# Performance work log

Measured on AMD Instinct MI355X. Metric: run time of the kernel, lower is better.

## Reference

```python
import jax, jax.numpy as jnp
import numpy as np

B, V, K, DIN, H, DH, OBS, HID = 2048, 3, 32, 256, 8, 64, 128, 256
REP = H * DH
EPS = 1e-6


def _ln(x, g, b):
    mu = x.mean(-1, keepdims=True)
    var = ((x - mu) ** 2).mean(-1, keepdims=True)
    return (x - mu) * jax.lax.rsqrt(var + 1e-5) * g + b


def setup_inputs() -> dict:
    key = jax.random.key(0)
    ks = iter(jax.random.split(key, 32))
    nrm = lambda shape, s=0.05: jax.random.normal(next(ks), shape, jnp.float32) * s
    return {
        'x_anchor': jax.random.normal(next(ks), (B, V, DIN), jnp.float32),
        'x_neighbors': jax.random.normal(next(ks), (B, V, K, DIN), jnp.float32),
        'edge_weights': jax.random.uniform(next(ks), (B, V, K), jnp.float32),
        'g': jax.random.normal(next(ks), (B, OBS), jnp.float32),
        'aW': nrm((V, DIN, REP)), 'ab': jnp.zeros((V, REP)), 'ag': jnp.ones((V, REP)), 'abeta': jnp.zeros((V, REP)),
        'nW': nrm((V, DIN, REP)), 'nb': jnp.zeros((V, REP)), 'ng': jnp.ones((V, REP)), 'nbeta': jnp.zeros((V, REP)),
        'Wq': nrm((V, H, DH, DH)), 'Wk': nrm((V, H, DH, DH)), 'Wv': nrm((V, H, DH, DH)), 'Wo': nrm((V, H, DH, DH)),
        'geom_log_scale': jnp.zeros((V, H)),
        'cWq': nrm((H, DH, DH)), 'cWk': nrm((H, DH, DH)), 'cWv': nrm((H, DH, DH)), 'cWo': nrm((H, DH, DH)),
        'rW1': nrm((OBS, HID)), 'rb1': jnp.zeros((HID,)),
        'rW2': nrm((HID, HID)), 'rb2': jnp.zeros((HID,)),
        'vW': nrm((HID, H * V)), 'vb': jnp.zeros((H * V,)),
        'mW': nrm((HID, H)), 'mb': jnp.zeros((H,)),
        'gW': nrm((HID, H)), 'gb': jnp.zeros((H,)),
    }


def reference(x_anchor, x_neighbors, edge_weights, g, aW, ab, ag, abeta, nW, nb, ng, nbeta,
              Wq, Wk, Wv, Wo, geom_log_scale, cWq, cWk, cWv, cWo,
              rW1, rb1, rW2, rb2, vW, vb, mW, mb, gW, gb):
    # --- per-view encoders (vectorized over V with a leading v axis) ---
    ha = _ln(jnp.einsum('bvi,vio->bvo', x_anchor, aW) + ab, ag, abeta).reshape(B, V, H, DH)
    hn = _ln(jnp.einsum('bvki,vio->bvko', x_neighbors, nW) + nb[:, None, :],
             ng[:, None, :], nbeta[:, None, :]).reshape(B, V, K, H, DH)
    q = jnp.einsum('bvhd,vhde->bvhe', ha, Wq)
    k = jnp.einsum('bvkhd,vhde->bvkhe', hn, Wk)
    vv = jnp.einsum('bvkhd,vhde->bvkhe', hn, Wv)
    sc = jnp.einsum('bvhd,bvkhd->bvhk', q, k) / np.sqrt(DH).astype(np.float32)
    geom = jax.nn.softplus(geom_log_scale)  # [V,H]
    sc = sc + geom[None, :, :, None] * jnp.log(edge_weights[:, :, None, :] + EPS)
    attn = jax.nn.softmax(sc, axis=-1)
    ho = jnp.einsum('bvhk,bvkhd->bvhd', attn, vv)
    ho = jnp.einsum('bvhd,vhde->bvhe', ho, Wo) + ha  # residual
    view_tokens = jnp.transpose(ho, (0, 2, 1, 3))  # [B,H,V,Dh]
    # --- router ---
    hid = jax.nn.gelu(jnp.dot(g, rW1) + rb1, approximate=False)
    hid = jax.nn.gelu(jnp.dot(hid, rW2) + rb2, approximate=False)
    pi = jax.nn.softmax((jnp.dot(hid, vW) + vb).reshape(B, H, V), axis=-1)
    beta = jax.nn.sigmoid((jnp.dot(hid, mW) + mb)[..., None])  # [B,H,1]
    gate = jax.nn.softmax(jnp.dot(hid, gW) + gb, axis=-1)      # [B,H]
    # --- pi-weighted mixture + cross-view interaction with log-pi prior ---
    mix = jnp.einsum('bhv,bhvd->bhd', pi, view_tokens)
    qc = jnp.einsum('bhd,hde->bhe', mix, cWq)
    kc = jnp.einsum('bhvd,hde->bhve', view_tokens, cWk)
    vc = jnp.einsum('bhvd,hde->bhve', view_tokens, cWv)
    s2 = jnp.einsum('bhd,bhvd->bhv', qc, kc) / np.sqrt(DH).astype(np.float32) + jnp.log(pi + EPS)
    a2 = jax.nn.softmax(s2, axis=-1)
    cr = jnp.einsum('bhv,bhvd->bhd', a2, vc)
    cr = jnp.einsum('bhd,hde->bhe', cr, cWo)
    # mode blend + head gating; head_repr kept unflattened [B,H,Dh]
    return gate[..., None] * (beta * cr + (1.0 - beta) * mix)
```

## Files before the change

kernel.cpp:

```cpp
#include <hip/hip_runtime.h>

#define B_   2048
#define V_   3
#define K_   32
#define DIN_ 256
#define H_   8
#define DH_  64
#define REP_ 512

typedef unsigned short u16;
typedef unsigned int   u32;
typedef __bf16 bf8 __attribute__((ext_vector_type(8)));
typedef float  f4  __attribute__((ext_vector_type(4)));

static __device__ __forceinline__ u16 f2bf(float f) {
  union { float f; u32 i; } x; x.f = f;
  u32 r = (x.i + 0x7FFFu + ((x.i >> 16) & 1u)) >> 16;
  return (u16)r;
}
static __device__ __forceinline__ float bf2f(u16 u) {
  union { u32 i; float f; } x; x.i = ((u32)u) << 16;
  return x.f;
}
static __device__ __forceinline__ float bflo(u32 q) {
  union { u32 i; float f; } x; x.i = q << 16; return x.f;
}
static __device__ __forceinline__ float bfhi(u32 q) {
  union { u32 i; float f; } x; x.i = q & 0xffff0000u; return x.f;
}

static __device__ __forceinline__ void gl2lds16(const u16* g, u16* l) {
  __builtin_amdgcn_global_load_lds(
      (const __attribute__((address_space(1))) unsigned int*)(g),
      (__attribute__((address_space(3))) unsigned int*)(l), 16, 0, 0);
}

__global__ __launch_bounds__(256) void k0_prep(
    const float* __restrict__ nW, const float* __restrict__ aW,
    const float* __restrict__ Wv,
    u16* __restrict__ nWt, u16* __restrict__ aWt,
    u16* __restrict__ Wvt)
{
  int id = blockIdx.x * 256 + threadIdx.x;
  if (id < 393216) {
    int v  = id / 131072, r  = id % 131072;
    int kt = r / 16384,   r2 = r % 16384;
    int n  = r2 >> 5;
    int s  = (r2 >> 3) & 3;
    int m  = r2 & 7;
    int c  = s ^ ((n >> 1) & 3);
    int k  = kt * 32 + c * 8 + m;
    int src = (v * 256 + k) * 512 + n;
    nWt[id] = f2bf(nW[src]);
    aWt[id] = f2bf(aW[src]);
  } else {
    int j = id - 393216;
    int vh = j / 4096, r = j % 4096;
    int e = r / 64, d = r % 64;
    int src = (vh * 64 + d) * 64 + e;
    Wvt[j] = f2bf(Wv[src]);
  }
}

__global__ __launch_bounds__(256) void k0_wqk(
    const float* __restrict__ Wq, const float* __restrict__ Wk,
    float* __restrict__ Wqk)
{
  int vh = blockIdx.x, t = threadIdx.x;
  __shared__ float wq[4096], wkT[4096];
  #pragma unroll
  for (int i = 0; i < 16; ++i) {
    int idx = i * 256 + t;
    wq[idx] = Wq[(long)vh * 4096 + idx];
    int e = idx >> 6, c = idx & 63;
    wkT[c * 64 + e] = Wk[(long)vh * 4096 + e * 64 + c];
  }
  __syncthreads();
  int d = t >> 2, e0 = (t & 3) * 16;
  float acc[16];
  #pragma unroll
  for (int j = 0; j < 16; ++j) acc[j] = 0.f;
  for (int c = 0; c < 64; ++c) {
    float a = wq[d * 64 + c];
    const float* wr = &wkT[c * 64 + e0];
    #pragma unroll
    for (int j = 0; j < 16; ++j) acc[j] += a * wr[j];
  }
  #pragma unroll
  for (int j = 0; j < 16; ++j) Wqk[(long)vh * 4096 + d * 64 + e0 + j] = acc[j];
}

union K1Smem {
  struct { u16 A[64 * 256]; u16 B[16384]; } p;
  u16 S[64 * 512];
};

__global__ __launch_bounds__(512, 4) void k1_gemm_ln(
    const float* __restrict__ X,
    const u16*   __restrict__ Wt,
    const float* __restrict__ bias,
    const float* __restrict__ gamma,
    const float* __restrict__ betap,
    u16*   __restrict__ hn,
    float* __restrict__ ha,
    int mode, int b0, int Bc)
{
  __shared__ K1Smem sm;
  const int v = blockIdx.y, blk = blockIdx.x, t = threadIdx.x;
  const int w = t >> 6, l = t & 63, lm = l & 15, lg = l >> 4;
  const int wm = w & 1, wn = w >> 1;

  float bcol[8];
  #pragma unroll
  for (int tn = 0; tn < 8; ++tn) bcol[tn] = bias[v * 512 + wn * 128 + tn * 16 + lm];

  {
    int row = t >> 3;
    int cbase = (t & 7) * 32;
    long grow;
    if (mode == 0) { int b = b0 + blk * 2 + (row >> 5); grow = ((long)(b * 3 + v) * 32 + (row & 31)) * 256; }
    else           { int b = blk * 64 + row;            grow = (long)(b * 3 + v) * 256; }
    const float4* src = (const float4*)(X + grow + cbase);
    int sw = row & 7;
    #pragma unroll
    for (int j = 0; j < 8; ++j) {
      float4 f = src[j];
      int col = cbase + j * 4;
      int c = col >> 3, m = col & 7;
      ushort4 u;
      u.x = f2bf(f.x); u.y = f2bf(f.y); u.z = f2bf(f.z); u.w = f2bf(f.w);
      *(ushort4*)&sm.p.A[row * 256 + ((c ^ sw) << 3) + m] = u;
    }
  }

  f4 acc[2][8];
  #pragma unroll
  for (int i = 0; i < 2; ++i)
    #pragma unroll
    for (int j = 0; j < 8; ++j) { f4 z = {0.f, 0.f, 0.f, 0.f}; acc[i][j] = z; }

  const u16* Wbase = Wt + (long)v * 8 * 16384;
  for (int kt = 0; kt < 8; ++kt) {
    __syncthreads();
    {
      const u16* gp = Wbase + (long)kt * 16384 + t * 8;
      u16* lp = &sm.p.B[t * 8];
      #pragma unroll
      for (int r = 0; r < 4; ++r) gl2lds16(gp + r * 4096, lp + r * 4096);
    }
    __syncthreads();
    bf8 af[2];
    #pragma unroll
    for (int tm = 0; tm < 2; ++tm) {
      int row = wm * 32 + tm * 16 + lm;
      int c = kt * 4 + lg;
      af[tm] = *(const bf8*)&sm.p.A[row * 256 + ((c ^ (row & 7)) << 3)];
    }
    #pragma unroll
    for (int tn = 0; tn < 8; ++tn) {
      int n = wn * 128 + tn * 16 + lm;
      bf8 bv = *(const bf8*)&sm.p.B[n * 32 + ((lg ^ ((n >> 1) & 3)) << 3)];
      acc[0][tn] = __builtin_amdgcn_mfma_f32_16x16x32_bf16(af[0], bv, acc[0][tn], 0, 0, 0);
      acc[1][tn] = __builtin_amdgcn_mfma_f32_16x16x32_bf16(af[1], bv, acc[1][tn], 0, 0, 0);
    }
  }
  __syncthreads();

  #pragma unroll
  for (int tm = 0; tm < 2; ++tm)
    #pragma unroll
    for (int tn = 0; tn < 8; ++tn) {
      int col = wn * 128 + tn * 16 + lm;
      int c = col >> 3, m = col & 7;
      #pragma unroll
      for (int r = 0; r < 4; ++r) {
        int row = wm * 32 + tm * 16 + lg * 4 + r;
        sm.S[row * 512 + ((c ^ (row & 7)) << 3) + m] = f2bf(acc[tm][tn][r] + bcol[tn]);
      }
    }
  __syncthreads();

  {
    int row = t >> 3, ch = t & 7, sw = row & 7;
    float s1 = 0.f, s2 = 0.f;
    #pragma unroll
    for (int j = 0; j < 8; ++j) {
      int c = j * 8 + ch;
      uint4 q = *(const uint4*)&sm.S[row * 512 + ((c ^ sw) << 3)];
      float x0 = bflo(q.x), x1 = bfhi(q.x), x2 = bflo(q.y), x3 = bfhi(q.y);
      float x4 = bflo(q.z), x5 = bfhi(q.z), x6 = bflo(q.w), x7 = bfhi(q.w);
      s1 += ((x0 + x1) + (x2 + x3)) + ((x4 + x5) + (x6 + x7));
      s2 += ((x0*x0 + x1*x1) + (x2*x2 + x3*x3)) + ((x4*x4 + x5*x5) + (x6*x6 + x7*x7));
    }
    #pragma unroll
    for (int d = 1; d < 8; d <<= 1) { s1 += __shfl_xor(s1, d, 64); s2 += __shfl_xor(s2, d, 64); }
    float mu = s1 * (1.f / 512.f);
    float var = s2 * (1.f / 512.f) - mu * mu;
    float rs = rsqrtf(var + 1e-5f);
    #pragma unroll
    for (int j = 0; j < 8; ++j) {
      int c = j * 8 + ch;
      uint4 q = *(const uint4*)&sm.S[row * 512 + ((c ^ sw) << 3)];
      int col0 = c * 8;
      float4 g0 = *(const float4*)&gamma[v * 512 + col0];
      float4 g1 = *(const float4*)&gamma[v * 512 + col0 + 4];
      float4 e0 = *(const float4*)&betap[v * 512 + col0];
      float4 e1 = *(const float4*)&betap[v * 512 + col0 + 4];
      float y0 = (bflo(q.x) - mu) * rs * g0.x + e0.x;
      float y1 = (bfhi(q.x) - mu) * rs * g0.y + e0.y;
      float y2 = (bflo(q.y) - mu) * rs * g0.z + e0.z;
      float y3 = (bfhi(q.y) - mu) * rs * g0.w + e0.w;
      float y4 = (bflo(q.z) - mu) * rs * g1.x + e1.x;
      float y5 = (bfhi(q.z) - mu) * rs * g1.y + e1.y;
      float y6 = (bflo(q.w) - mu) * rs * g1.z + e1.z;
      float y7 = (bfhi(q.w) - mu) * rs * g1.w + e1.w;
      if (mode == 0) {
        uint4 q4;
        q4.x = (u32)f2bf(y0) | ((u32)f2bf(y1) << 16);
        q4.y = (u32)f2bf(y2) | ((u32)f2bf(y3) << 16);
        q4.z = (u32)f2bf(y4) | ((u32)f2bf(y5) << 16);
        q4.w = (u32)f2bf(y6) | ((u32)f2bf(y7) << 16);
        int bl_ = blk * 2 + (row >> 5), krow = row & 31;
        u16* dst = hn + (((long)(v * 8 + j) * Bc + bl_) * 32 + krow) * 64 + ch * 8;
        *(uint4*)dst = q4;
      } else {
        int b = blk * 64 + row;
        float* dst = ha + (long)(b * 3 + v) * 512 + col0;
        float4 w0, w1;
        w0.x = y0; w0.y = y1; w0.z = y2; w0.w = y3;
        w1.x = y4; w1.y = y5; w1.z = y6; w1.w = y7;
        *(float4*)dst = w0;
        *(float4*)(dst + 4) = w1;
      }
    }
  }
}

__global__ __launch_bounds__(256, 2) void k2_attn(
    const u16*   __restrict__ hn,
    const float* __restrict__ ha,
    const u16*   __restrict__ Wvt,
    const float* __restrict__ Wqk,
    const float* __restrict__ Wo,
    const float* __restrict__ ew,
    const float* __restrict__ gls,
    float* __restrict__ vt,
    int b0, int Bc)
{
  const int v = blockIdx.z, h = blockIdx.y;
  const int bL0 = blockIdx.x * 4;
  const int t = threadIdx.x;
  __shared__ u16 A[128 * 72];
  __shared__ u16 Wv_s[64 * 72];
  __shared__ float t_s[4 * 64], ha_s[4 * 64], attn_s[4 * 32], o_s[4 * 64];

  {
    const uint4* src = (const uint4*)(hn + ((long)(v * 8 + h) * Bc + bL0) * 2048);
    int r = t >> 1, half = t & 1;
    #pragma unroll
    for (int i = 0; i < 4; ++i) {
      uint4 d = src[r * 8 + half * 4 + i];
      *(uint4*)&A[r * 72 + half * 32 + i * 8] = d;
    }
  }
  {
    const uint4* sv = (const uint4*)(Wvt + (long)(v * 8 + h) * 4096);
    #pragma unroll
    for (int i = 0; i < 2; ++i) {
      int idx = i * 256 + t;
      int n = idx >> 3, k8 = (idx & 7) * 8;
      *(uint4*)&Wv_s[n * 72 + k8] = sv[idx];
    }
  }
  {
    int b = t >> 6, e = t & 63;
    ha_s[t] = ha[((long)(b0 + bL0 + b) * 3 + v) * 512 + h * 64 + e];
  }
  __syncthreads();

  const int w = t >> 6, l = t & 63, lm = l & 15, lg = l >> 4;
  f4 aV[2][4];
  #pragma unroll
  for (int i = 0; i < 2; ++i)
    #pragma unroll
    for (int j = 0; j < 4; ++j) { f4 z = {0.f, 0.f, 0.f, 0.f}; aV[i][j] = z; }

  #pragma unroll
  for (int ks = 0; ks < 2; ++ks) {
    int ko = ks * 32 + lg * 8;
    bf8 af[2];
    #pragma unroll
    for (int tm = 0; tm < 2; ++tm) af[tm] = *(const bf8*)&A[(w * 32 + tm * 16 + lm) * 72 + ko];
    #pragma unroll
    for (int tn = 0; tn < 4; ++tn) {
      bf8 bv = *(const bf8*)&Wv_s[(tn * 16 + lm) * 72 + ko];
      #pragma unroll
      for (int tm = 0; tm < 2; ++tm)
        aV[tm][tn] = __builtin_amdgcn_mfma_f32_16x16x32_bf16(af[tm], bv, aV[tm][tn], 0, 0, 0);
    }
  }

  {
    const float* wqk = Wqk + (long)(v * 8 + h) * 4096;
    int b = t >> 6, e = t & 63;
    float acc = 0.f;
    for (int d = 0; d < 64; ++d) acc += ha_s[b * 64 + d] * wqk[d * 64 + e];
    t_s[t] = acc * 0.125f;
  }
  __syncthreads();

  if (t < 128) {
    int b = t >> 5, k = t & 31;
    float x = gls[v * 8 + h];
    float gsc = (x > 20.f) ? x : log1pf(expf(x));
    float s = 0.f;
    const u16* kr = &A[(b * 32 + k) * 72];
    const float* tb = &t_s[b * 64];
    #pragma unroll
    for (int j = 0; j < 8; ++j) {
      uint4 q = *(const uint4*)(kr + j * 8);
      const float* tj = tb + j * 8;
      s += tj[0] * bflo(q.x) + tj[1] * bfhi(q.x)
         + tj[2] * bflo(q.y) + tj[3] * bfhi(q.y)
         + tj[4] * bflo(q.z) + tj[5] * bfhi(q.z)
         + tj[6] * bflo(q.w) + tj[7] * bfhi(q.w);
    }
    float e_w = ew[((long)(b0 + bL0 + b) * 3 + v) * 32 + k];
    s += gsc * logf(e_w + 1e-6f);
    float m = s;
    #pragma unroll
    for (int d = 1; d < 32; d <<= 1) m = fmaxf(m, __shfl_xor(m, d, 64));
    float exs = expf(s - m), sum = exs;
    #pragma unroll
    for (int d = 1; d < 32; d <<= 1) sum += __shfl_xor(sum, d, 64);
    attn_s[b * 32 + k] = exs / sum;
  }
  __syncthreads();

  {
    float p[4] = {0.f, 0.f, 0.f, 0.f};
    #pragma unroll
    for (int tm = 0; tm < 2; ++tm)
      #pragma unroll
      for (int r = 0; r < 4; ++r) {
        int k = tm * 16 + lg * 4 + r;
        float a = attn_s[w * 32 + k];
        #pragma unroll
        for (int tn = 0; tn < 4; ++tn) p[tn] += a * aV[tm][tn][r];
      }
    #pragma unroll
    for (int tn = 0; tn < 4; ++tn) {
      float x = p[tn];
      x += __shfl_xor(x, 16, 64);
      x += __shfl_xor(x, 32, 64);
      if (l < 16) o_s[w * 64 + tn * 16 + lm] = x;
    }
  }
  __syncthreads();

  {
    const float* wo = Wo + (long)(v * 8 + h) * 4096;
    int b = t >> 6, e = t & 63;
    float acc = ha_s[b * 64 + e];
    for (int d = 0; d < 64; ++d) acc += o_s[b * 64 + d] * wo[d * 64 + e];
    vt[(((long)(b0 + bL0 + b) * 8 + h) * 3 + v) * 64 + e] = acc;
  }
}

__global__ __launch_bounds__(256) void k3_router(
    const float* __restrict__ g, const float* __restrict__ rW1, const float* __restrict__ rb1,
    const float* __restrict__ rW2, const float* __restrict__ rb2,
    const float* __restrict__ vW, const float* __restrict__ vb,
    const float* __restrict__ mW, const float* __restrict__ mb,
    const float* __restrict__ gW, const float* __restrict__ gb,
    float* __restrict__ pi, float* __restrict__ beta_o, float* __restrict__ gate_o)
{
  __shared__ float gs[4 * 128], h1[4 * 256], h2[4 * 256], lgt[4 * 40];
  int t = threadIdx.x, bb = blockIdx.x * 4;
  #pragma unroll
  for (int r = 0; r < 2; ++r) { int idx = r * 256 + t; gs[idx] = g[(long)bb * 128 + idx]; }
  __syncthreads();
  {
    int bl = t >> 6, e0 = (t & 63) * 4;
    float acc[4];
    #pragma unroll
    for (int j = 0; j < 4; ++j) acc[j] = rb1[e0 + j];
    for (int i = 0; i < 128; ++i) {
      float gv = gs[bl * 128 + i];
      const float* wr = rW1 + i * 256 + e0;
      #pragma unroll
      for (int j = 0; j < 4; ++j) acc[j] += gv * wr[j];
    }
    #pragma unroll
    for (int j = 0; j < 4; ++j) { float x = acc[j]; h1[bl * 256 + e0 + j] = 0.5f * x * (1.f + erff(x * 0.70710678118f)); }
  }
  __syncthreads();
  {
    int bl = t >> 6, e0 = (t & 63) * 4;
    float acc[4];
    #pragma unroll
    for (int j = 0; j < 4; ++j) acc[j] = rb2[e0 + j];
    for (int i = 0; i < 256; ++i) {
      float hv = h1[bl * 256 + i];
      const float* wr = rW2 + i * 256 + e0;
      #pragma unroll
      for (int j = 0; j < 4; ++j) acc[j] += hv * wr[j];
    }
    #pragma unroll
    for (int j = 0; j < 4; ++j) { float x = acc[j]; h2[bl * 256 + e0 + j] = 0.5f * x * (1.f + erff(x * 0.70710678118f)); }
  }
  __syncthreads();
  if (t < 160) {
    int bl = t / 40, j = t % 40;
    const float* W; float bs; int col, stride;
    if (j < 24)      { W = vW; col = j;      stride = 24; bs = vb[j]; }
    else if (j < 32) { W = mW; col = j - 24; stride = 8;  bs = mb[j - 24]; }
    else             { W = gW; col = j - 32; stride = 8;  bs = gb[j - 32]; }
    float acc = bs;
    for (int i = 0; i < 256; ++i) acc += h2[bl * 256 + i] * W[i * stride + col];
    lgt[bl * 40 + j] = acc;
  }
  __syncthreads();
  if (t < 4) {
    int b = bb + t;
    const float* L = &lgt[t * 40];
    #pragma unroll
    for (int hh = 0; hh < 8; ++hh) {
      float a0 = L[hh * 3], a1 = L[hh * 3 + 1], a2v = L[hh * 3 + 2];
      float m = fmaxf(a0, fmaxf(a1, a2v));
      float x0 = expf(a0 - m), x1 = expf(a1 - m), x2 = expf(a2v - m);
      float inv = 1.f / (x0 + x1 + x2);
      pi[b * 24 + hh * 3 + 0] = x0 * inv;
      pi[b * 24 + hh * 3 + 1] = x1 * inv;
      pi[b * 24 + hh * 3 + 2] = x2 * inv;
      beta_o[b * 8 + hh] = 1.f / (1.f + expf(-L[24 + hh]));
    }
    float m = L[32];
    #pragma unroll
    for (int hh = 1; hh < 8; ++hh) m = fmaxf(m, L[32 + hh]);
    float s = 0.f, ex[8];
    #pragma unroll
    for (int hh = 0; hh < 8; ++hh) { ex[hh] = expf(L[32 + hh] - m); s += ex[hh]; }
    float inv = 1.f / s;
    #pragma unroll
    for (int hh = 0; hh < 8; ++hh) gate_o[b * 8 + hh] = ex[hh] * inv;
  }
}

__global__ __launch_bounds__(256) void k4_cross(
    const float* __restrict__ vtg, const float* __restrict__ pig,
    const float* __restrict__ betag, const float* __restrict__ gateg,
    const float* __restrict__ cWq, const float* __restrict__ cWk,
    const float* __restrict__ cWv, const float* __restrict__ cWo,
    float* __restrict__ out)
{
  __shared__ float smem[12544];
  float* vts   = smem;
  float* mixs  = smem + 6144;
  float* buf1  = smem + 8192;
  float* buf2  = smem + 10240;
  float* a2s   = smem + 12288;
  float* pis   = smem + 12384;
  float* betas = smem + 12480;
  float* gates = smem + 12512;

  int t = threadIdx.x, bblk = blockIdx.x * 4;
  {
    const float4* src = (const float4*)(vtg + (long)bblk * 1536);
    #pragma unroll
    for (int r = 0; r < 6; ++r) ((float4*)vts)[r * 256 + t] = src[r * 256 + t];
    if (t < 96) pis[t] = pig[bblk * 24 + t];
    if (t < 32) { betas[t] = betag[bblk * 8 + t]; gates[t] = gateg[bblk * 8 + t]; }
  }
  __syncthreads();
  int bl = t >> 6, hh = (t >> 3) & 7, e0 = (t & 7) * 8;
  const float* vbh = &vts[(bl * 8 + hh) * 192];
  {
    float p0 = pis[bl * 24 + hh * 3], p1 = pis[bl * 24 + hh * 3 + 1], p2 = pis[bl * 24 + hh * 3 + 2];
    #pragma unroll
    for (int j = 0; j < 8; ++j) {
      int e = e0 + j;
      mixs[(bl * 8 + hh) * 64 + e] = p0 * vbh[e] + p1 * vbh[64 + e] + p2 * vbh[128 + e];
    }
  }
  __syncthreads();
  {
    float acc[8] = {0.f,0.f,0.f,0.f,0.f,0.f,0.f,0.f};
    const float* M = &mixs[(bl * 8 + hh) * 64];
    for (int d = 0; d < 64; ++d) {
      float mv = M[d];
      const float* wr = &cWq[(hh * 64 + d) * 64 + e0];
      #pragma unroll
      for (int j = 0; j < 8; ++j) acc[j] += mv * wr[j];
    }
    #pragma unroll
    for (int j = 0; j < 8; ++j) buf1[(bl * 8 + hh) * 64 + e0 + j] = acc[j] * 0.125f;
  }
  __syncthreads();
  {
    const float* Q = &buf1[(bl * 8 + hh) * 64];
    #pragma unroll
    for (int d2 = 0; d2 < 8; ++d2) {
      const float* wr = &cWk[(hh * 64 + e0 + d2) * 64];
      float a = 0.f;
      for (int e = 0; e < 64; ++e) a += wr[e] * Q[e];
      buf2[(bl * 8 + hh) * 64 + e0 + d2] = a;
    }
  }
  __syncthreads();
  if (t < 32) {
    int b2 = t >> 3, h2 = t & 7;
    const float* Wd = &buf2[(b2 * 8 + h2) * 64];
    const float* vb2 = &vts[(b2 * 8 + h2) * 192];
    float s[3];
    #pragma unroll
    for (int v3 = 0; v3 < 3; ++v3) {
      float a = 0.f;
      for (int d = 0; d < 64; ++d) a += Wd[d] * vb2[v3 * 64 + d];
      s[v3] = a + logf(pis[b2 * 24 + h2 * 3 + v3] + 1e-6f);
    }
    float m = fmaxf(s[0], fmaxf(s[1], s[2]));
    float x0 = expf(s[0] - m), x1 = expf(s[1] - m), x2 = expf(s[2] - m);
    float inv = 1.f / (x0 + x1 + x2);
    a2s[(b2 * 8 + h2) * 3 + 0] = x0 * inv;
    a2s[(b2 * 8 + h2) * 3 + 1] = x1 * inv;
    a2s[(b2 * 8 + h2) * 3 + 2] = x2 * inv;
  }
  __syncthreads();
  {
    float a0 = a2s[(bl * 8 + hh) * 3], a1 = a2s[(bl * 8 + hh) * 3 + 1], a2v = a2s[(bl * 8 + hh) * 3 + 2];
    #pragma unroll
    for (int j = 0; j < 8; ++j) {
      int e = e0 + j;
      buf1[(bl * 8 + hh) * 64 + e] = a0 * vbh[e] + a1 * vbh[64 + e] + a2v * vbh[128 + e];
    }
  }
  __syncthreads();
  {
    float acc[8] = {0.f,0.f,0.f,0.f,0.f,0.f,0.f,0.f};
    const float* Y = &buf1[(bl * 8 + hh) * 64];
    for (int d = 0; d < 64; ++d) {
      float yv = Y[d];
      const float* wr = &cWv[(hh * 64 + d) * 64 + e0];
      #pragma unroll
      for (int j = 0; j < 8; ++j) acc[j] += yv * wr[j];
    }
    #pragma unroll
    for (int j = 0; j < 8; ++j) buf2[(bl * 8 + hh) * 64 + e0 + j] = acc[j];
  }
  __syncthreads();
  {
    float acc[8] = {0.f,0.f,0.f,0.f,0.f,0.f,0.f,0.f};
    const float* C2 = &buf2[(bl * 8 + hh) * 64];
    for (int d = 0; d < 64; ++d) {
      float cv = C2[d];
      const float* wr = &cWo[(hh * 64 + d) * 64 + e0];
      #pragma unroll
      for (int j = 0; j < 8; ++j) acc[j] += cv * wr[j];
    }
    float bt = betas[bl * 8 + hh], gt = gates[bl * 8 + hh];
    const float* M = &mixs[(bl * 8 + hh) * 64];
    #pragma unroll
    for (int j = 0; j < 8; ++j)
      out[((long)(bblk + bl) * 8 + hh) * 64 + e0 + j] = gt * (bt * acc[j] + (1.f - bt) * M[e0 + j]);
  }
}

extern "C" void kernel_launch(void* const* d_in, const int* in_sizes, int n_in,
                              void* d_out, int out_size, void* d_ws, size_t ws_size,
                              hipStream_t stream) {
  const float* x_anchor    = (const float*)d_in[0];
  const float* x_neighbors = (const float*)d_in[1];
  const float* edge_w      = (const float*)d_in[2];
  const float* g           = (const float*)d_in[3];
  const float* aW  = (const float*)d_in[4];
  const float* ab  = (const float*)d_in[5];
  const float* ag  = (const float*)d_in[6];
  const float* abeta = (const float*)d_in[7];
  const float* nW  = (const float*)d_in[8];
  const float* nb  = (const float*)d_in[9];
  const float* ng  = (const float*)d_in[10];
  const float* nbeta = (const float*)d_in[11];
  const float* Wq  = (const float*)d_in[12];
  const float* Wk  = (const float*)d_in[13];
  const float* Wv  = (const float*)d_in[14];
  const float* Wo  = (const float*)d_in[15];
  const float* gls = (const float*)d_in[16];
  const float* cWq = (const float*)d_in[17];
  const float* cWk = (const float*)d_in[18];
  const float* cWv = (const float*)d_in[19];
  const float* cWo = (const float*)d_in[20];
  const float* rW1 = (const float*)d_in[21];
  const float* rb1 = (const float*)d_in[22];
  const float* rW2 = (const float*)d_in[23];
  const float* rb2 = (const float*)d_in[24];
  const float* vW  = (const float*)d_in[25];
  const float* vb  = (const float*)d_in[26];
  const float* mW  = (const float*)d_in[27];
  const float* mb  = (const float*)d_in[28];
  const float* gW  = (const float*)d_in[29];
  const float* gb  = (const float*)d_in[30];

  char* p = (char*)d_ws;
  u16* nWt = (u16*)p;  p += 786432;
  u16* aWt = (u16*)p;  p += 786432;
  u16* Wvt = (u16*)p;  p += 196608;
  float* WqkB = (float*)p; p += 393216;
  float* ha   = (float*)p; p += 12582912;
  float* vtb  = (float*)p; p += 12582912;
  float* pib  = (float*)p; p += 196608;
  float* betb = (float*)p; p += 65536;
  float* gatb = (float*)p; p += 65536;
  size_t fixed = (size_t)(p - (char*)d_ws);
  int C = 1;
  while (C < 128 && fixed + (size_t)(2048 / C) * 98304 > ws_size) C <<= 1;
  int Bc = 2048 / C;
  u16* hnb = (u16*)p;

  k0_prep<<<1920, 256, 0, stream>>>(nW, aW, Wv, nWt, aWt, Wvt);
  k0_wqk<<<24, 256, 0, stream>>>(Wq, Wk, WqkB);
  k1_gemm_ln<<<dim3(32, 3), 512, 0, stream>>>(x_anchor, aWt, ab, ag, abeta,
                                              (u16*)nullptr, ha, 1, 0, Bc);
  k3_router<<<512, 256, 0, stream>>>(g, rW1, rb1, rW2, rb2, vW, vb, mW, mb, gW, gb,
                                     pib, betb, gatb);
  for (int c = 0; c < C; ++c) {
    int b0 = c * Bc;
    k1_gemm_ln<<<dim3(Bc / 2, 3), 512, 0, stream>>>(x_neighbors, nWt, nb, ng, nbeta,
                                                    hnb, (float*)nullptr, 0, b0, Bc);
    k2_attn<<<dim3(Bc / 4, 8, 3), 256, 0, stream>>>(hnb, ha, Wvt, WqkB, Wo,
                                                    edge_w, gls, vtb, b0, Bc);
  }
  k4_cross<<<512, 256, 0, stream>>>(vtb, pib, betb, gatb, cWq, cWk, cWv, cWo,
                                    (float*)d_out);
}
```

Measured before the change: 749.6 us.

## Fuse neighbor GEMM+LayerNorm with per-head attention into one kernel

Merges the neighbor encoder GEMM+LayerNorm kernel and the attention kernel into a single kernel. Each block keeps the normalized 64x512 neighbor tile for two batch rows in shared memory and runs all eight heads' score, softmax, value projection and output projection on it. This removes the bf16 hn round-trip through global memory and the chunked launch loop. The cost is much larger shared memory per block, which lowers occupancy. Wv is now read straight from global memory rather than staged, and the Wqk/Wo loops are serialized across heads per thread.

```diff
diff --git a/kernel.cpp b/kernel.cpp
--- a/kernel.cpp
+++ b/kernel.cpp
@@ -236,96 +236,181 @@
   }
 }
 
-__global__ __launch_bounds__(256, 2) void k2_attn(
-    const u16*   __restrict__ hn,
+__global__ __launch_bounds__(512, 4) void k12_fused(
+    const float* __restrict__ X,
+    const u16*   __restrict__ Wt,
+    const float* __restrict__ bias,
+    const float* __restrict__ gamma,
+    const float* __restrict__ betap,
     const float* __restrict__ ha,
     const u16*   __restrict__ Wvt,
     const float* __restrict__ Wqk,
     const float* __restrict__ Wo,
     const float* __restrict__ ew,
     const float* __restrict__ gls,
-    float* __restrict__ vt,
-    int b0, int Bc)
+    float* __restrict__ vt)
 {
-  const int v = blockIdx.z, h = blockIdx.y;
-  const int bL0 = blockIdx.x * 4;
-  const int t = threadIdx.x;
-  __shared__ u16 A[128 * 72];
-  __shared__ u16 Wv_s[64 * 72];
-  __shared__ float t_s[4 * 64], ha_s[4 * 64], attn_s[4 * 32], o_s[4 * 64];
-
-  {
-    const uint4* src = (const uint4*)(hn + ((long)(v * 8 + h) * Bc + bL0) * 2048);
-    int r = t >> 1, half = t & 1;
-    #pragma unroll
-    for (int i = 0; i < 4; ++i) {
-      uint4 d = src[r * 8 + half * 4 + i];
-      *(uint4*)&A[r * 72 + half * 32 + i * 8] = d;
-    }
-  }
-  {
-    const uint4* sv = (const uint4*)(Wvt + (long)(v * 8 + h) * 4096);
-    #pragma unroll
-    for (int i = 0; i < 2; ++i) {
-      int idx = i * 256 + t;
-      int n = idx >> 3, k8 = (idx & 7) * 8;
-      *(uint4*)&Wv_s[n * 72 + k8] = sv[idx];
-    }
-  }
-  {
-    int b = t >> 6, e = t & 63;
-    ha_s[t] = ha[((long)(b0 + bL0 + b) * 3 + v) * 512 + h * 64 + e];
-  }
-  __syncthreads();
-
+  __shared__ K1Smem sm;
+  __shared__ float tS[1024];
+  __shared__ float aS[512];
+  __shared__ float oS[1024];
+  __shared__ float haS[1024];
+
+  const int v = blockIdx.y, blk = blockIdx.x, t = threadIdx.x;
   const int w = t >> 6, l = t & 63, lm = l & 15, lg = l >> 4;
-  f4 aV[2][4];
+  const int wm = w & 1, wn = w >> 1;
+
+  float bcol[8];
+  #pragma unroll
+  for (int tn = 0; tn < 8; ++tn) bcol[tn] = bias[v * 512 + wn * 128 + tn * 16 + lm];
+
+  {
+    int row = t >> 3;
+    int cbase = (t & 7) * 32;
+    int b = blk * 2 + (row >> 5);
+    long grow = ((long)(b * 3 + v) * 32 + (row & 31)) * 256;
+    const float4* src = (const float4*)(X + grow + cbase);
+    int sw = row & 7;
+    #pragma unroll
+    for (int j = 0; j < 8; ++j) {
+      float4 f = src[j];
+      int col = cbase + j * 4;
+      int c = col >> 3, m = col & 7;
+      ushort4 u;
+      u.x = f2bf(f.x); u.y = f2bf(f.y); u.z = f2bf(f.z); u.w = f2bf(f.w);
+      *(ushort4*)&sm.p.A[row * 256 + ((c ^ sw) << 3) + m] = u;
+    }
+  }
+  {
+    int b = t >> 8, e = (t & 255) * 2;
+    *(float2*)&haS[b * 512 + e] =
+        *(const float2*)&ha[((long)(blk * 2 + b) * 3 + v) * 512 + e];
+  }
+
+  f4 acc[2][8];
   #pragma unroll
   for (int i = 0; i < 2; ++i)
     #pragma unroll
-    for (int j = 0; j < 4; ++j) { f4 z = {0.f, 0.f, 0.f, 0.f}; aV[i][j] = z; }
-
-  #pragma unroll
-  for (int ks = 0; ks < 2; ++ks) {
-    int ko = ks * 32 + lg * 8;
+    for (int j = 0; j < 8; ++j) { f4 z = {0.f, 0.f, 0.f, 0.f}; acc[i][j] = z; }
+
+  const u16* Wbase = Wt + (long)v * 8 * 16384;
+  for (int kt = 0; kt < 8; ++kt) {
+    __syncthreads();
+    {
+      const u16* gp = Wbase + (long)kt * 16384 + t * 8;
+      u16* lp = &sm.p.B[t * 8];
+      #pragma unroll
+      for (int r = 0; r < 4; ++r) gl2lds16(gp + r * 4096, lp + r * 4096);
+    }
+    __syncthreads();
     bf8 af[2];
     #pragma unroll
-    for (int tm = 0; tm < 2; ++tm) af[tm] = *(const bf8*)&A[(w * 32 + tm * 16 + lm) * 72 + ko];
-    #pragma unroll
-    for (int tn = 0; tn < 4; ++tn) {
-      bf8 bv = *(const bf8*)&Wv_s[(tn * 16 + lm) * 72 + ko];
-      #pragma unroll
-      for (int tm = 0; tm < 2; ++tm)
-        aV[tm][tn] = __builtin_amdgcn_mfma_f32_16x16x32_bf16(af[tm], bv, aV[tm][tn], 0, 0, 0);
-    }
-  }
-
-  {
-    const float* wqk = Wqk + (long)(v * 8 + h) * 4096;
-    int b = t >> 6, e = t & 63;
-    float acc = 0.f;
-    for (int d = 0; d < 64; ++d) acc += ha_s[b * 64 + d] * wqk[d * 64 + e];
-    t_s[t] = acc * 0.125f;
-  }
-  __syncthreads();
-
-  if (t < 128) {
-    int b = t >> 5, k = t & 31;
+    for (int tm = 0; tm < 2; ++tm) {
+      int row = wm * 32 + tm * 16 + lm;
+      int c = kt * 4 + lg;
+      af[tm] = *(const bf8*)&sm.p.A[row * 256 + ((c ^ (row & 7)) << 3)];
+    }
+    #pragma unroll
+    for (int tn = 0; tn < 8; ++tn) {
+      int n = wn * 128 + tn * 16 + lm;
+      bf8 bv = *(const bf8*)&sm.p.B[n * 32 + ((lg ^ ((n >> 1) & 3)) << 3)];
+      acc[0][tn] = __builtin_amdgcn_mfma_f32_16x16x32_bf16(af[0], bv, acc[0][tn], 0, 0, 0);
+      acc[1][tn] = __builtin_amdgcn_mfma_f32_16x16x32_bf16(af[1], bv, acc[1][tn], 0, 0, 0);
+    }
+  }
+  __syncthreads();
+
+  #pragma unroll
+  for (int tm = 0; tm < 2; ++tm)
+    #pragma unroll
+    for (int tn = 0; tn < 8; ++tn) {
+      int col = wn * 128 + tn * 16 + lm;
+      int c = col >> 3, m = col & 7;
+      #pragma unroll
+      for (int r = 0; r < 4; ++r) {
+        int row = wm * 32 + tm * 16 + lg * 4 + r;
+        sm.S[row * 512 + ((c ^ (row & 7)) << 3) + m] = f2bf(acc[tm][tn][r] + bcol[tn]);
+      }
+    }
+  __syncthreads();
+
+  {
+    int row = t >> 3, ch = t & 7, sw = row & 7;
+    float s1 = 0.f, s2 = 0.f;
+    #pragma unroll
+    for (int j = 0; j < 8; ++j) {
+      int c = j * 8 + ch;
+      uint4 q = *(const uint4*)&sm.S[row * 512 + ((c ^ sw) << 3)];
+      float x0 = bflo(q.x), x1 = bfhi(q.x), x2 = bflo(q.y), x3 = bfhi(q.y);
+      float x4 = bflo(q.z), x5 = bfhi(q.z), x6 = bflo(q.w), x7 = bfhi(q.w);
+      s1 += ((x0 + x1) + (x2 + x3)) + ((x4 + x5) + (x6 + x7));
+      s2 += ((x0*x0 + x1*x1) + (x2*x2 + x3*x3)) + ((x4*x4 + x5*x5) + (x6*x6 + x7*x7));
+    }
+    #pragma unroll
+    for (int d = 1; d < 8; d <<= 1) { s1 += __shfl_xor(s1, d, 64); s2 += __shfl_xor(s2, d, 64); }
+    float mu = s1 * (1.f / 512.f);
+    float var = s2 * (1.f / 512.f) - mu * mu;
+    float rs = rsqrtf(var + 1e-5f);
+    #pragma unroll
+    for (int j = 0; j < 8; ++j) {
+      int c = j * 8 + ch;
+      u16* sp = &sm.S[row * 512 + ((c ^ sw) << 3)];
+      uint4 q = *(const uint4*)sp;
+      int col0 = c * 8;
+      float4 g0 = *(const float4*)&gamma[v * 512 + col0];
+      float4 g1 = *(const float4*)&gamma[v * 512 + col0 + 4];
+      float4 e0 = *(const float4*)&betap[v * 512 + col0];
+      float4 e1 = *(const float4*)&betap[v * 512 + col0 + 4];
+      float y0 = (bflo(q.x) - mu) * rs * g0.x + e0.x;
+      float y1 = (bfhi(q.x) - mu) * rs * g0.y + e0.y;
+      float y2 = (bflo(q.y) - mu) * rs * g0.z + e0.z;
+      float y3 = (bfhi(q.y) - mu) * rs * g0.w + e0.w;
+      float y4 = (bflo(q.z) - mu) * rs * g1.x + e1.x;
+      float y5 = (bfhi(q.z) - mu) * rs * g1.y + e1.y;
+      float y6 = (bflo(q.w) - mu) * rs * g1.z + e1.z;
+      float y7 = (bfhi(q.w) - mu) * rs * g1.w + e1.w;
+      uint4 q4;
+      q4.x = (u32)f2bf(y0) | ((u32)f2bf(y1) << 16);
+      q4.y = (u32)f2bf(y2) | ((u32)f2bf(y3) << 16);
+      q4.z = (u32)f2bf(y4) | ((u32)f2bf(y5) << 16);
+      q4.w = (u32)f2bf(y6) | ((u32)f2bf(y7) << 16);
+      *(uint4*)sp = q4;
+    }
+  }
+  {
+    int h = t >> 6, e = t & 63;
+    const float* wq = Wqk + (long)(v * 8 + h) * 4096;
+    float a0 = 0.f, a1 = 0.f;
+    const float* h0 = &haS[h * 64];
+    const float* h1 = &haS[512 + h * 64];
+    for (int d = 0; d < 64; ++d) {
+      float wv = wq[d * 64 + e];
+      a0 += h0[d] * wv;
+      a1 += h1[d] * wv;
+    }
+    tS[h * 64 + e]       = a0 * 0.125f;
+    tS[512 + h * 64 + e] = a1 * 0.125f;
+  }
+  __syncthreads();
+
+  {
+    int b = t >> 8, h = (t >> 5) & 7, k = t & 31;
     float x = gls[v * 8 + h];
     float gsc = (x > 20.f) ? x : log1pf(expf(x));
+    int r = b * 32 + k, sw = r & 7;
+    const float* tb = &tS[(b * 8 + h) * 64];
     float s = 0.f;
-    const u16* kr = &A[(b * 32 + k) * 72];
-    const float* tb = &t_s[b * 64];
-    #pragma unroll
-    for (int j = 0; j < 8; ++j) {
-      uint4 q = *(const uint4*)(kr + j * 8);
+    #pragma unroll
+    for (int j = 0; j < 8; ++j) {
+      int c8 = h * 8 + j;
+      uint4 q = *(const uint4*)&sm.S[r * 512 + ((c8 ^ sw) << 3)];
       const float* tj = tb + j * 8;
       s += tj[0] * bflo(q.x) + tj[1] * bfhi(q.x)
          + tj[2] * bflo(q.y) + tj[3] * bfhi(q.y)
          + tj[4] * bflo(q.z) + tj[5] * bfhi(q.z)
          + tj[6] * bflo(q.w) + tj[7] * bfhi(q.w);
     }
-    float e_w = ew[((long)(b0 + bL0 + b) * 3 + v) * 32 + k];
+    float e_w = ew[((long)(blk * 2 + b) * 3 + v) * 32 + k];
     s += gsc * logf(e_w + 1e-6f);
     float m = s;
     #pragma unroll
@@ -333,37 +418,70 @@
     float exs = expf(s - m), sum = exs;
     #pragma unroll
     for (int d = 1; d < 32; d <<= 1) sum += __shfl_xor(sum, d, 64);
-    attn_s[b * 32 + k] = exs / sum;
-  }
-  __syncthreads();
-
-  {
-    float p[4] = {0.f, 0.f, 0.f, 0.f};
+    aS[(b * 8 + h) * 32 + k] = exs / sum;
+  }
+  __syncthreads();
+
+  for (int i = 0; i < 2; ++i) {
+    int p = w * 2 + i, b = p >> 3, h = p & 7;
+    const u16* wvg = Wvt + (long)(v * 8 + h) * 4096;
+    f4 aV[2][4];
+    #pragma unroll
+    for (int a = 0; a < 2; ++a)
+      #pragma unroll
+      for (int j = 0; j < 4; ++j) { f4 z = {0.f, 0.f, 0.f, 0.f}; aV[a][j] = z; }
+    #pragma unroll
+    for (int ks = 0; ks < 2; ++ks) {
+      int ko = ks * 32 + lg * 8;
+      bf8 af[2];
+      #pragma unroll
+      for (int tm = 0; tm < 2; ++tm) {
+        int r = b * 32 + tm * 16 + lm;
+        int c8 = h * 8 + ks * 4 + lg;
+        af[tm] = *(const bf8*)&sm.S[r * 512 + ((c8 ^ (r & 7)) << 3)];
+      }
+      #pragma unroll
+      for (int tn = 0; tn < 4; ++tn) {
+        bf8 bv = *(const bf8*)&wvg[(tn * 16 + lm) * 64 + ko];
+        #pragma unroll
+        for (int tm = 0; tm < 2; ++tm)
+          aV[tm][tn] = __builtin_amdgcn_mfma_f32_16x16x32_bf16(af[tm], bv, aV[tm][tn], 0, 0, 0);
+      }
+    }
+    float pp[4] = {0.f, 0.f, 0.f, 0.f};
     #pragma unroll
     for (int tm = 0; tm < 2; ++tm)
       #pragma unroll
-      for (int r = 0; r < 4; ++r) {
-        int k = tm * 16 + lg * 4 + r;
-        float a = attn_s[w * 32 + k];
+      for (int r4 = 0; r4 < 4; ++r4) {
+        int k = tm * 16 + lg * 4 + r4;
+        float a = aS[p * 32 + k];
         #pragma unroll
-        for (int tn = 0; tn < 4; ++tn) p[tn] += a * aV[tm][tn][r];
+        for (int tn = 0; tn < 4; ++tn) pp[tn] += a * aV[tm][tn][r4];
       }
     #pragma unroll
     for (int tn = 0; tn < 4; ++tn) {
-      float x = p[tn];
+      float x = pp[tn];
       x += __shfl_xor(x, 16, 64);
       x += __shfl_xor(x, 32, 64);
-      if (l < 16) o_s[w * 64 + tn * 16 + lm] = x;
-    }
-  }
-  __syncthreads();
-
-  {
+      if (l < 16) oS[p * 64 + tn * 16 + lm] = x;
+    }
+  }
+  __syncthreads();
+
+  {
+    int h = t >> 6, e = t & 63;
     const float* wo = Wo + (long)(v * 8 + h) * 4096;
-    int b = t >> 6, e = t & 63;
-    float acc = ha_s[b * 64 + e];
-    for (int d = 0; d < 64; ++d) acc += o_s[b * 64 + d] * wo[d * 64 + e];
-    vt[(((long)(b0 + bL0 + b) * 8 + h) * 3 + v) * 64 + e] = acc;
+    float a0 = haS[h * 64 + e];
+    float a1 = haS[512 + h * 64 + e];
+    const float* o0 = &oS[h * 64];
+    const float* o1 = &oS[512 + h * 64];
+    for (int d = 0; d < 64; ++d) {
+      float wv = wo[d * 64 + e];
+      a0 += o0[d] * wv;
+      a1 += o1[d] * wv;
+    }
+    vt[(((long)(blk * 2 + 0) * 8 + h) * 3 + v) * 64 + e] = a0;
+    vt[(((long)(blk * 2 + 1) * 8 + h) * 3 + v) * 64 + e] = a1;
   }
 }
 
@@ -611,25 +729,16 @@
   float* pib  = (float*)p; p += 196608;
   float* betb = (float*)p; p += 65536;
   float* gatb = (float*)p; p += 65536;
-  size_t fixed = (size_t)(p - (char*)d_ws);
-  int C = 1;
-  while (C < 128 && fixed + (size_t)(2048 / C) * 98304 > ws_size) C <<= 1;
-  int Bc = 2048 / C;
-  u16* hnb = (u16*)p;
+  (void)ws_size;
 
   k0_prep<<<1920, 256, 0, stream>>>(nW, aW, Wv, nWt, aWt, Wvt);
   k0_wqk<<<24, 256, 0, stream>>>(Wq, Wk, WqkB);
   k1_gemm_ln<<<dim3(32, 3), 512, 0, stream>>>(x_anchor, aWt, ab, ag, abeta,
-                                              (u16*)nullptr, ha, 1, 0, Bc);
+                                              (u16*)nullptr, ha, 1, 0, 2048);
   k3_router<<<512, 256, 0, stream>>>(g, rW1, rb1, rW2, rb2, vW, vb, mW, mb, gW, gb,
                                      pib, betb, gatb);
-  for (int c = 0; c < C; ++c) {
-    int b0 = c * Bc;
-    k1_gemm_ln<<<dim3(Bc / 2, 3), 512, 0, stream>>>(x_neighbors, nWt, nb, ng, nbeta,
-                                                    hnb, (float*)nullptr, 0, b0, Bc);
-    k2_attn<<<dim3(Bc / 4, 8, 3), 256, 0, stream>>>(hnb, ha, Wvt, WqkB, Wo,
-                                                    edge_w, gls, vtb, b0, Bc);
-  }
+  k12_fused<<<dim3(1024, 3), 512, 0, stream>>>(x_neighbors, nWt, nb, ng, nbeta,
+                                               ha, Wvt, WqkB, Wo, edge_w, gls, vtb);
   k4_cross<<<512, 256, 0, stream>>>(vtb, pib, betb, gatb, cWq, cWk, cWv, cWo,
                                     (float*)d_out);
 }
```

New measurement: 815.8 us. 8.8% more time.
